# Performance work log

Measured on AMD Instinct MI355X. Metric: run time of the kernel, lower is better.

## Reference

```python
import jax, jax.numpy as jnp
import numpy as np

B, J, V, G, D = 1, 24, 20000, 2, 3
DCIN = J * 12          # num_parts * (9 + 3)
DC = 4                 # d_cond
HID = 128
BETA = 100.0           # softplus beta
EPS = 1e-8


def softplus_b(x):
    return jax.nn.softplus(BETA * x) / BETA


def group_linear(x, W, b):
    # x: (J, N, din), W: (J, din, dout), b: (J, dout)
    return jnp.einsum('jnd,jdo->jno', x, W) + b[:, None, :]


def axis_angle_to_matrix(aa):
    # aa: (..., 3) -> (..., 3, 3), Rodrigues formula
    angle = jnp.linalg.norm(aa, axis=-1, keepdims=True)
    axis = aa / jnp.where(angle < 1e-12, 1.0, angle)
    x, y, z = axis[..., 0], axis[..., 1], axis[..., 2]
    a = angle[..., 0]
    c, s = jnp.cos(a), jnp.sin(a)
    C = 1.0 - c
    r0 = jnp.stack([c + x * x * C, x * y * C - z * s, x * z * C + y * s], axis=-1)
    r1 = jnp.stack([y * x * C + z * s, c + y * y * C, y * z * C - x * s], axis=-1)
    r2 = jnp.stack([z * x * C - y * s, z * y * C + x * s, c + z * z * C], axis=-1)
    return jnp.stack([r0, r1, r2], axis=-2)


def blending_weights(pts, Jtr_center, Jtr_neigh, Jtr_self, bid_this, bid_other, rigid_alpha, rigid_beta):
    # pts: (B,J,V,3); Jtr_*: (B,J,1,3); bid_*: (J,) int
    ra = jax.nn.elu(rigid_alpha - 1.0) + 1.0
    a_n = ra[bid_other, bid_this].reshape(1, -1, 1, 1)
    a_s = ra[bid_this, bid_other].reshape(1, -1, 1, 1)
    be_n = rigid_beta[bid_other, bid_this].reshape(1, -1, 1, 1)
    be_s = rigid_beta[bid_this, bid_other].reshape(1, -1, 1, 1)
    vec_bone_n = Jtr_neigh - Jtr_center
    vec_bone_s = Jtr_self - Jtr_center
    nb_n = jnp.linalg.norm(vec_bone_n, axis=-1, keepdims=True)
    nb_s = jnp.linalg.norm(vec_bone_s, axis=-1, keepdims=True)
    vb_n = (Jtr_neigh - Jtr_self) / (nb_n + nb_s + EPS) * nb_n
    vb_s = -vb_n / (nb_n + EPS) * nb_s
    n_n = jnp.linalg.norm(vb_n, axis=-1, keepdims=True)
    n_s = jnp.linalg.norm(vb_s, axis=-1, keepdims=True)
    tr_o = Jtr_neigh - vb_n
    vec_pts = jax.lax.stop_gradient(pts) - tr_o   # pts.detach() in torch
    d_n = vb_n / (n_n + EPS)
    d_s = vb_s / (n_s + EPS)
    r_n = jnp.sum(vec_pts * d_n, axis=-1, keepdims=True) / (n_n + EPS)
    r_s = jnp.sum(vec_pts * d_s, axis=-1, keepdims=True) / (n_s + EPS)
    return jax.nn.sigmoid((r_n * a_n + be_n) - (r_s * a_s + be_s))


def _forward(pts, Bcond, Btr, Brot, Bneigh, rigid_alpha, rigid_beta,
             cW0, cb0, cW1, cb1, cW2, cb2, W0, b0, W1, b1, W2, b2, W3, b3):
    # world -> per-part local coords: (B,J,V,3)
    Brot_inv = jnp.swapaxes(Brot, -1, -2)
    pts_local = jnp.einsum('bjxy,bjvy->bjvx', Brot_inv, pts[:, None] - Btr[:, :, None])
    # neighbor-based deformation offsets
    ids = jax.lax.stop_gradient(Bneigh[0, :, :, 4, :2]).astype(jnp.int32)  # (J,G,2)
    offset_sum = jnp.zeros_like(pts_local)
    for gi in range(G):  # small fixed neighbor count
        Jtr_this = Bneigh[:, :, gi, 0][:, :, None]    # (B,J,1,3)
        Jtr_center = Bneigh[:, :, gi, 1][:, :, None]
        Jtr_other = Bneigh[:, :, gi, 2][:, :, None]
        Jpose = Bneigh[:, :, gi, 3][:, :, None]
        w = blending_weights(pts_local, Jtr_center, Jtr_other, Jtr_this,
                             ids[:, gi, 0], ids[:, gi, 1], rigid_alpha, rigid_beta)  # (B,J,V,1)
        Jp_w = jnp.nan_to_num(Jpose * w)              # (B,J,V,3)
        R = axis_angle_to_matrix(-Jp_w)               # (B,J,V,3,3)
        off = jnp.einsum('bjvxy,bjvy->bjvx', R, pts_local - Jtr_center) + Jtr_center - pts_local
        offset_sum = offset_sum + jnp.nan_to_num(off)
    pts_local = pts_local + offset_sum
    # grouped per-part MLP (INR with num_groups=J)
    x_in = jnp.transpose(pts_local, (1, 0, 2, 3)).reshape(J, B * V, D)
    cond = jnp.broadcast_to(jnp.transpose(Bcond, (1, 0, 2))[:, :, None, :], (J, B, V, DCIN)).reshape(J, B * V, DCIN)
    c = softplus_b(group_linear(cond, cW0, cb0))
    c = softplus_b(group_linear(c, cW1, cb1))
    c = group_linear(c, cW2, cb2)                      # (J, BV, 4)
    x = jnp.concatenate([x_in, c], axis=-1)            # (J, BV, 7)
    x = softplus_b(group_linear(x, W0, b0))
    x = softplus_b(group_linear(x, W1, b1))
    x = softplus_b(group_linear(x, W2, b2))
    x = group_linear(x, W3, b3)                        # (J, BV, 1)
    pred_parts = jnp.transpose(x.reshape(J, B, V, 1), (1, 0, 2, 3))  # (B,J,V,1)
    # softmin blend over parts
    pred_min = jnp.min(pred_parts, axis=1)             # (B,V,1)
    delta = pred_parts - pred_min[:, None]
    wsm = jax.nn.softmax(-delta * 200.0, axis=1)       # Softmin(dim=1)
    return jnp.sum(delta * wsm, axis=1) + pred_min


def setup_inputs() -> dict:
    key = jax.random.key(0)
    ks = jax.random.split(key, 16)
    pts = jax.random.normal(ks[0], (B, V, D), jnp.float32)
    Bcond = jax.random.normal(ks[1], (B, J, DCIN), jnp.float32) * 0.1
    Btr = jax.random.normal(ks[2], (B, J, D), jnp.float32)
    Brot = jax.random.normal(ks[3], (B, J, D, D), jnp.float32)
    core = jax.random.normal(ks[4], (B, J, G, 4, D), jnp.float32) * 0.5
    ids_this = jnp.arange(J, dtype=jnp.float32)
    ids_o0 = jnp.mod(jnp.arange(J) + 1, J).astype(jnp.float32)
    ids_o1 = jnp.mod(jnp.arange(J) - 1, J).astype(jnp.float32)
    bid = jnp.zeros((B, J, G, 1, D), jnp.float32)
    bid = bid.at[:, :, 0, 0, 0].set(ids_this).at[:, :, 0, 0, 1].set(ids_o0)
    bid = bid.at[:, :, 1, 0, 0].set(ids_this).at[:, :, 1, 0, 1].set(ids_o1)
    Bneigh = jnp.concatenate([core, bid], axis=-2)     # (B,J,G,5,D)
    rigid_alpha = jnp.full((J, J), 2.0, jnp.float32)   # blend_alpha init
    rigid_beta = jnp.zeros((J, J), jnp.float32)
    def gl(k, din, dout, std):
        return jax.random.normal(k, (J, din, dout), jnp.float32) * std, jnp.zeros((J, dout), jnp.float32)
    cW0, cb0 = gl(ks[5], DCIN, DC * 4, float(np.sqrt(2.0 / DCIN)))
    cW1, cb1 = gl(ks[6], DC * 4, DC * 4, float(np.sqrt(2.0 / (DC * 4))))
    cW2, cb2 = gl(ks[7], DC * 4, DC, 1e-5)
    std_h = float(np.sqrt(2.0) / np.sqrt(HID))
    W0, b0 = gl(ks[8], D + DC, HID, std_h)
    W1, b1 = gl(ks[9], HID, HID, std_h)
    W2, b2 = gl(ks[10], HID, HID, std_h)
    W3 = jax.random.normal(ks[11], (J, HID, 1), jnp.float32) * 1e-5 + float(np.sqrt(np.pi) / np.sqrt(HID))
    b3 = jnp.full((J, 1), -1.0, jnp.float32)           # -radius_init
    return {'pts': pts, 'Bcond': Bcond, 'Btr': Btr, 'Brot': Brot, 'Bneigh': Bneigh,
            'rigid_alpha': rigid_alpha, 'rigid_beta': rigid_beta,
            'cW0': cW0, 'cb0': cb0, 'cW1': cW1, 'cb1': cb1, 'cW2': cW2, 'cb2': cb2,
            'W0': W0, 'b0': b0, 'W1': W1, 'b1': b1, 'W2': W2, 'b2': b2, 'W3': W3, 'b3': b3}


def reference(pts, Bcond, Btr, Brot, Bneigh, rigid_alpha, rigid_beta,
              cW0, cb0, cW1, cb1, cW2, cb2, W0, b0, W1, b1, W2, b2, W3, b3):
    return _forward(pts, Bcond, Btr, Brot, Bneigh, rigid_alpha, rigid_beta,
                    cW0, cb0, cW1, cb1, cW2, cb2, W0, b0, W1, b1, W2, b2, W3, b3)
```

## Files before the change

### kernel.cpp

```cpp
#include <hip/hip_runtime.h>
#include <hip/hip_bf16.h>
#include <math.h>

#define VN 20000
#define JN 24
#define TILE 64
#define KP 132
#define EPSF 1e-8f

typedef __attribute__((ext_vector_type(8))) short bfrag;
typedef __attribute__((ext_vector_type(4))) float f32x4;

#define WJ_STRIDE 73728
#define L0H 0
#define L0L 4096
#define L1H 8192
#define L1L 24576
#define L2H 40960
#define L2L 57344

__device__ __forceinline__ unsigned short f2bf(float x) {
    __hip_bfloat16 b = __float2bfloat16(x);
    unsigned short u; __builtin_memcpy(&u, &b, 2); return u;
}
__device__ __forceinline__ float bf2f(unsigned short u) {
    __hip_bfloat16 b; __builtin_memcpy(&b, &u, 2);
    return __bfloat162float(b);
}
__device__ __forceinline__ unsigned int pack_hl(float x) {
    const unsigned int ux = __float_as_uint(x) + 0x8000u;
    const unsigned int h  = ux & 0xffff0000u;
    const float lo = x - __uint_as_float(h);
    const unsigned int ul = __float_as_uint(lo) + 0x8000u;
    return (h >> 16) | (ul & 0xffff0000u);
}

__device__ __forceinline__ float softplus_fast(float x) {
    const float u = __expf(-100.0f * fabsf(x));
    const float y = 2.0f * u - 1.0f;
    float p = fmaf(y, 0.0009515f, -0.0034665f);
    p = fmaf(y, p, 0.0122786f);
    p = fmaf(y, p, -0.0554079f);
    p = fmaf(y, p, 0.3333420f);
    p = fmaf(y, p, 0.4054545f);
    return fmaf(0.01f, p, fmaxf(x, 0.0f));
}

__global__ __launch_bounds__(384) void prep_kernel(
    const float* __restrict__ Bcond, const float* __restrict__ Bneigh,
    const float* __restrict__ ralpha, const float* __restrict__ rbeta,
    const float* __restrict__ cW0, const float* __restrict__ cb0,
    const float* __restrict__ cW1, const float* __restrict__ cb1,
    const float* __restrict__ cW2, const float* __restrict__ cb2,
    float* __restrict__ c4, float* __restrict__ geom)
{
    __shared__ float hbuf[JN][16];
    const int t = threadIdx.x;

    if (t < JN * 2) {
        const int j = t >> 1, gi = t & 1;
        const float* nb = Bneigh + (j * 2 + gi) * 15;
        const float tx = nb[0],  ty = nb[1],  tz = nb[2];
        const float cx = nb[3],  cy = nb[4],  cz = nb[5];
        const float ox = nb[6],  oy = nb[7],  oz = nb[8];
        const float px = nb[9],  py = nb[10], pz = nb[11];
        const int bid_this  = (int)nb[12];
        const int bid_other = (int)nb[13];
        const float xa_n = ralpha[bid_other * JN + bid_this] - 1.0f;
        const float xa_s = ralpha[bid_this * JN + bid_other] - 1.0f;
        const float a_n = xa_n > 0.0f ? xa_n + 1.0f : expf(xa_n);
        const float a_s = xa_s > 0.0f ? xa_s + 1.0f : expf(xa_s);
        const float be_n = rbeta[bid_other * JN + bid_this];
        const float be_s = rbeta[bid_this * JN + bid_other];

        const float bnx = ox - cx, bny = oy - cy, bnz = oz - cz;
        const float bsx = tx - cx, bsy = ty - cy, bsz = tz - cz;
        const float nb_n = sqrtf(bnx*bnx + bny*bny + bnz*bnz);
        const float nb_s = sqrtf(bsx*bsx + bsy*bsy + bsz*bsz);
        const float f = nb_n / (nb_n + nb_s + EPSF);
        const float vbnx = (ox - tx) * f, vbny = (oy - ty) * f, vbnz = (oz - tz) * f;
        const float g2 = -nb_s / (nb_n + EPSF);
        const float vbsx = vbnx * g2, vbsy = vbny * g2, vbsz = vbnz * g2;
        const float n_n = sqrtf(vbnx*vbnx + vbny*vbny + vbnz*vbnz);
        const float n_s = sqrtf(vbsx*vbsx + vbsy*vbsy + vbsz*vbsz);
        const float trx = ox - vbnx, tr_y = oy - vbny, trz = oz - vbnz;
        const float inn = 1.0f / ((n_n + EPSF) * (n_n + EPSF));
        const float ins = 1.0f / ((n_s + EPSF) * (n_s + EPSF));
        const float gx = vbnx * inn * a_n - vbsx * ins * a_s;
        const float gy = vbny * inn * a_n - vbsy * ins * a_s;
        const float gz = vbnz * inn * a_n - vbsz * ins * a_s;
        const float h = -(trx * gx + tr_y * gy + trz * gz) + be_n - be_s;
        float* gm = geom + (j * 2 + gi) * 12;
        gm[0] = gx; gm[1] = gy; gm[2] = gz; gm[3] = h;
        gm[4] = px; gm[5] = py; gm[6] = pz;
        gm[7] = cx; gm[8] = cy; gm[9] = cz;
        gm[10] = 0.0f; gm[11] = 0.0f;
    }

    {
        const int j = t >> 4, o = t & 15;
        const float* cond = Bcond + j * 288;
        const float* w = cW0 + j * 288 * 16 + o;
        float acc = cb0[j * 16 + o];
        for (int d = 0; d < 288; ++d) acc = fmaf(cond[d], w[d * 16], acc);
        hbuf[j][o] = softplus_fast(acc);
    }
    __syncthreads();
    {
        const int j = t >> 4, o = t & 15;
        const float* w = cW1 + j * 256 + o;
        float acc = cb1[j * 16 + o];
        #pragma unroll
        for (int d = 0; d < 16; ++d) acc = fmaf(hbuf[j][d], w[d * 16], acc);
        acc = softplus_fast(acc);
        __syncthreads();
        hbuf[j][o] = acc;
    }
    __syncthreads();
    if (t < JN * 4) {
        const int j = t >> 2, o = t & 3;
        const float* w = cW2 + j * 64 + o;
        float acc = cb2[j * 4 + o];
        #pragma unroll
        for (int d = 0; d < 16; ++d) acc = fmaf(hbuf[j][d], w[d * 4], acc);
        c4[j * 4 + o] = acc;
    }
}

__global__ __launch_bounds__(256) void wprep_kernel(
    const float* __restrict__ W0, const float* __restrict__ W1,
    const float* __restrict__ W2, unsigned short* __restrict__ wt)
{
    const int g = blockIdx.x * 256 + threadIdx.x;
    const int jj = g / 36864;
    const int r = g - jj * 36864;
    const float* src; int idx, kin, hoff, loff;
    if (r < 4096)       { idx = r;         kin = 7;   src = W0 + jj * 896;   hoff = L0H; loff = L0L; }
    else if (r < 20480) { idx = r - 4096;  kin = 128; src = W1 + jj * 16384; hoff = L1H; loff = L1L; }
    else                { idx = r - 20480; kin = 128; src = W2 + jj * 16384; hoff = L2H; loff = L2L; }
    const int j8   = idx & 7;
    const int lane = (idx >> 3) & 63;
    const int nt   = (idx >> 9) & 7;
    const int ks   = idx >> 12;
    const int n = nt * 16 + (lane & 15);
    const int k = ks * 32 + (lane >> 4) * 8 + j8;
    const float v = (k < kin) ? src[k * 128 + n] : 0.0f;
    const unsigned short h = f2bf(v);
    const unsigned short l = f2bf(v - bf2f(h));
    unsigned short* dj = wt + jj * WJ_STRIDE;
    dj[hoff + idx] = h;
    dj[loff + idx] = l;
}

__device__ __forceinline__ void mfma_layer(
    unsigned int* __restrict__ X,
    const unsigned short* __restrict__ wh,
    const unsigned short* __restrict__ wl,
    const float* __restrict__ bvec,
    int q, int lane, int nks)
{
    const int l = lane & 15;
    const int quad = lane >> 4;
    const float bia0 = bvec[q * 32 + l];
    const float bia1 = bvec[q * 32 + 16 + l];
    f32x4 acc[4][2];
    #pragma unroll
    for (int mi = 0; mi < 4; ++mi) {
        acc[mi][0] = (f32x4){bia0, bia0, bia0, bia0};
        acc[mi][1] = (f32x4){bia1, bia1, bia1, bia1};
    }

    #pragma unroll 1
    for (int ks = 0; ks < nks; ++ks) {
        bfrag bh[2], bl[2];
        #pragma unroll
        for (int ni = 0; ni < 2; ++ni) {
            const int off = ((ks * 8 + (q * 2 + ni)) * 64 + lane) * 8;
            bh[ni] = *(const bfrag*)(wh + off);
            bl[ni] = *(const bfrag*)(wl + off);
        }
        #pragma unroll
        for (int mi = 0; mi < 4; ++mi) {
            const unsigned int* ap = X + (mi * 16 + l) * KP + ks * 32 + quad * 8;
            union { uint4 v[2]; unsigned int u[8]; } d;
            d.v[0] = *(const uint4*)ap;
            d.v[1] = *(const uint4*)(ap + 4);
            union { unsigned int u[4]; bfrag f; } ah, al;
            #pragma unroll
            for (int jj = 0; jj < 4; ++jj) {
                ah.u[jj] = __builtin_amdgcn_perm(d.u[2*jj+1], d.u[2*jj], 0x05040100u);
                al.u[jj] = __builtin_amdgcn_perm(d.u[2*jj+1], d.u[2*jj], 0x07060302u);
            }
            #pragma unroll
            for (int ni = 0; ni < 2; ++ni) {
                acc[mi][ni] = __builtin_amdgcn_mfma_f32_16x16x32_bf16(ah.f, bh[ni], acc[mi][ni], 0, 0, 0);
                acc[mi][ni] = __builtin_amdgcn_mfma_f32_16x16x32_bf16(al.f, bh[ni], acc[mi][ni], 0, 0, 0);
                acc[mi][ni] = __builtin_amdgcn_mfma_f32_16x16x32_bf16(ah.f, bl[ni], acc[mi][ni], 0, 0, 0);
            }
        }
    }
    __syncthreads();
    #pragma unroll
    for (int ni = 0; ni < 2; ++ni) {
        const int ch = q * 32 + ni * 16 + l;
        #pragma unroll
        for (int mi = 0; mi < 4; ++mi) {
            #pragma unroll
            for (int r = 0; r < 4; ++r) {
                const float v = softplus_fast(acc[mi][ni][r]);
                const int p = mi * 16 + quad * 4 + r;
                X[p * KP + ch] = pack_hl(v);
            }
        }
    }
    __syncthreads();
}

__global__ __launch_bounds__(256, 4) void main_kernel(
    const float* __restrict__ pts, const float* __restrict__ Btr,
    const float* __restrict__ Brot,
    const float* __restrict__ b0, const float* __restrict__ b1,
    const float* __restrict__ b2, const float* __restrict__ W3,
    const float* __restrict__ b3,
    const float* __restrict__ c4, const float* __restrict__ geom,
    const unsigned short* __restrict__ wt,
    float* __restrict__ pred)
{
    __shared__ unsigned int X[TILE * KP];
    const int j = blockIdx.y;
    const int v0 = blockIdx.x * TILE;
    const int t = threadIdx.x;
    const int lane = t & 63;
    const int q = __builtin_amdgcn_readfirstlane(t >> 6);

    if (t < TILE) {
        const int v = v0 + t;
        float plx = 0.0f, ply = 0.0f, plz = 0.0f;
        if (v < VN) {
            const float dx = pts[v * 3 + 0] - Btr[j * 3 + 0];
            const float dy = pts[v * 3 + 1] - Btr[j * 3 + 1];
            const float dz = pts[v * 3 + 2] - Btr[j * 3 + 2];
            const float* R = Brot + j * 9;
            plx = R[0] * dx + R[3] * dy + R[6] * dz;
            ply = R[1] * dx + R[4] * dy + R[7] * dz;
            plz = R[2] * dx + R[5] * dy + R[8] * dz;
            float osx = 0.0f, osy = 0.0f, osz = 0.0f;
            #pragma unroll
            for (int gi = 0; gi < 2; ++gi) {
                const float* gm = geom + (j * 2 + gi) * 12;
                const float arg = plx * gm[0] + ply * gm[1] + plz * gm[2] + gm[3];
                const float w = 1.0f / (1.0f + __expf(-arg));
                const float aax = -gm[4] * w, aay = -gm[5] * w, aaz = -gm[6] * w;
                const float jcx = gm[7], jcy = gm[8], jcz = gm[9];
                const float ang = sqrtf(aax * aax + aay * aay + aaz * aaz);
                const float inv = ang < 1e-12f ? 1.0f : 1.0f / ang;
                const float ux = aax * inv, uy = aay * inv, uz = aaz * inv;
                const float co = __cosf(ang), si = __sinf(ang), C = 1.0f - co;
                const float vx = plx - jcx, vy = ply - jcy, vz = plz - jcz;
                const float du = ux * vx + uy * vy + uz * vz;
                const float cxv = uy * vz - uz * vy;
                const float cyv = uz * vx - ux * vz;
                const float czv = ux * vy - uy * vx;
                float offx = co * vx + si * cxv + C * ux * du + jcx - plx;
                float offy = co * vy + si * cyv + C * uy * du + jcy - ply;
                float offz = co * vz + si * czv + C * uz * du + jcz - plz;
                if (isnan(offx)) offx = 0.0f;
                if (isnan(offy)) offy = 0.0f;
                if (isnan(offz)) offz = 0.0f;
                osx += offx; osy += offy; osz += offz;
            }
            plx += osx; ply += osy; plz += osz;
        }
        X[t * KP + 0] = pack_hl(plx);
        X[t * KP + 1] = pack_hl(ply);
        X[t * KP + 2] = pack_hl(plz);
        X[t * KP + 3] = pack_hl(c4[j * 4 + 0]);
        X[t * KP + 4] = pack_hl(c4[j * 4 + 1]);
        X[t * KP + 5] = pack_hl(c4[j * 4 + 2]);
        X[t * KP + 6] = pack_hl(c4[j * 4 + 3]);
        #pragma unroll
        for (int k = 7; k < 32; ++k) X[t * KP + k] = 0u;
    }
    __syncthreads();

    const unsigned short* wj = wt + j * WJ_STRIDE;
    mfma_layer(X, wj + L0H, wj + L0L, b0 + j * 128, q, lane, 1);
    mfma_layer(X, wj + L1H, wj + L1L, b1 + j * 128, q, lane, 4);
    mfma_layer(X, wj + L2H, wj + L2L, b2 + j * 128, q, lane, 4);

    {
        const float* w3 = W3 + j * 128 + q * 32;
        float part = 0.0f;
        #pragma unroll 8
        for (int kk = 0; kk < 32; ++kk) {
            const unsigned int d = X[lane * KP + q * 32 + kk];
            const float xv = __uint_as_float(d << 16)
                           + __uint_as_float(d & 0xffff0000u);
            part = fmaf(xv, w3[kk], part);
        }
        X[lane * KP + 128 + q] = __float_as_uint(part);
    }
    __syncthreads();
    if (t < TILE) {
        const int v = v0 + t;
        const float r = b3[j]
            + __uint_as_float(X[t * KP + 128]) + __uint_as_float(X[t * KP + 129])
            + __uint_as_float(X[t * KP + 130]) + __uint_as_float(X[t * KP + 131]);
        if (v < VN) pred[j * VN + v] = r;
    }
}

__global__ __launch_bounds__(256) void softmin_kernel(const float* __restrict__ pred,
                                                      float* __restrict__ out)
{
    const int v = blockIdx.x * 256 + threadIdx.x;
    if (v >= VN) return;
    float vals[JN];
    float m = 3.4e38f;
    #pragma unroll
    for (int jj = 0; jj < JN; ++jj) {
        vals[jj] = pred[jj * VN + v];
        m = fminf(m, vals[jj]);
    }
    float s1 = 0.0f, s2 = 0.0f;
    #pragma unroll
    for (int jj = 0; jj < JN; ++jj) {
        const float d = vals[jj] - m;
        const float e = __expf(-200.0f * d);
        s1 += e;
        s2 = fmaf(d, e, s2);
    }
    out[v] = s2 / s1 + m;
}

extern "C" void kernel_launch(void* const* d_in, const int* in_sizes, int n_in,
                              void* d_out, int out_size, void* d_ws, size_t ws_size,
                              hipStream_t stream)
{
    const float* pts    = (const float*)d_in[0];
    const float* Bcond  = (const float*)d_in[1];
    const float* Btr    = (const float*)d_in[2];
    const float* Brot   = (const float*)d_in[3];
    const float* Bneigh = (const float*)d_in[4];
    const float* ralpha = (const float*)d_in[5];
    const float* rbeta  = (const float*)d_in[6];
    const float* cW0 = (const float*)d_in[7];
    const float* cb0 = (const float*)d_in[8];
    const float* cW1 = (const float*)d_in[9];
    const float* cb1 = (const float*)d_in[10];
    const float* cW2 = (const float*)d_in[11];
    const float* cb2 = (const float*)d_in[12];
    const float* W0 = (const float*)d_in[13];
    const float* b0 = (const float*)d_in[14];
    const float* W1 = (const float*)d_in[15];
    const float* b1 = (const float*)d_in[16];
    const float* W2 = (const float*)d_in[17];
    const float* b2 = (const float*)d_in[18];
    const float* W3 = (const float*)d_in[19];
    const float* b3 = (const float*)d_in[20];

    float* ws   = (float*)d_ws;
    float* pred = ws;
    float* c4   = ws + JN * VN;
    float* geom = c4 + JN * 4;
    unsigned short* wt = (unsigned short*)(geom + JN * 2 * 12);

    prep_kernel<<<1, 384, 0, stream>>>(Bcond, Bneigh, ralpha, rbeta,
                                       cW0, cb0, cW1, cb1, cW2, cb2, c4, geom);

    wprep_kernel<<<(JN * 36864) / 256, 256, 0, stream>>>(W0, W1, W2, wt);

    dim3 grid((VN + TILE - 1) / TILE, JN);
    main_kernel<<<grid, 256, 0, stream>>>(pts, Btr, Brot,
                                          b0, b1, b2, W3, b3,
                                          c4, geom, wt, pred);

    softmin_kernel<<<(VN + 255) / 256, 256, 0, stream>>>(pred, (float*)d_out);
}
```

Baseline: 257.3 us.

## Fold split-bf16 activations into doubled K dimension, cutting MFMAs from three to two

Activations are kept as interleaved (hi, lo) bf16 pairs, so the A fragment is read straight from LDS with no perm unpacking. The weights are laid out with K doubled: one matrix holds the hi weight for both hi and lo activations, and a second holds the lo weight for the hi slot and zero for the lo slot. Each k-step now issues two MFMAs instead of three, but the K loop runs twice as many steps and the weight buffer is larger. Softplus is also rewritten with exp2 and a different polynomial, and the hi/lo packing now uses the v_cvt_pk_bf16_f32 instruction.

```diff
diff --git a/kernel.cpp b/kernel.cpp
--- a/kernel.cpp
+++ b/kernel.cpp
@@ -11,13 +11,13 @@
 typedef __attribute__((ext_vector_type(8))) short bfrag;
 typedef __attribute__((ext_vector_type(4))) float f32x4;
 
-#define WJ_STRIDE 73728
-#define L0H 0
-#define L0L 4096
-#define L1H 8192
-#define L1L 24576
-#define L2H 40960
-#define L2L 57344
+#define WJ_STRIDE 139264
+#define L0A 0
+#define L0B 4096
+#define L1A 8192
+#define L1B 40960
+#define L2A 73728
+#define L2B 106496
 
 __device__ __forceinline__ unsigned short f2bf(float x) {
     __hip_bfloat16 b = __float2bfloat16(x);
@@ -28,22 +28,22 @@
     return __bfloat162float(b);
 }
 __device__ __forceinline__ unsigned int pack_hl(float x) {
-    const unsigned int ux = __float_as_uint(x) + 0x8000u;
-    const unsigned int h  = ux & 0xffff0000u;
-    const float lo = x - __uint_as_float(h);
-    const unsigned int ul = __float_as_uint(lo) + 0x8000u;
-    return (h >> 16) | (ul & 0xffff0000u);
+    const unsigned int h = (__float_as_uint(x) + 0x8000u) & 0xffff0000u;
+    const float hf = __uint_as_float(h);
+    const float lo = x - hf;
+    unsigned int r;
+    asm("v_cvt_pk_bf16_f32 %0, %1, %2" : "=v"(r) : "v"(hf), "v"(lo));
+    return r;
 }
 
 __device__ __forceinline__ float softplus_fast(float x) {
-    const float u = __expf(-100.0f * fabsf(x));
-    const float y = 2.0f * u - 1.0f;
-    float p = fmaf(y, 0.0009515f, -0.0034665f);
-    p = fmaf(y, p, 0.0122786f);
-    p = fmaf(y, p, -0.0554079f);
-    p = fmaf(y, p, 0.3333420f);
-    p = fmaf(y, p, 0.4054545f);
-    return fmaf(0.01f, p, fmaxf(x, 0.0f));
+    const float u = __builtin_amdgcn_exp2f(-144.269504f * fabsf(x));
+    float p = fmaf(u, 3.04480e-4f, -1.31584e-3f);
+    p = fmaf(u, p, 2.852768e-3f);
+    p = fmaf(u, p, -4.902308e-3f);
+    p = fmaf(u, p, 9.992342e-3f);
+    p = fmaf(u, p, 8.0e-8f);
+    return fmaxf(x, 0.0f) + p;
 }
 
 __global__ __launch_bounds__(384) void prep_kernel(
@@ -132,30 +132,31 @@
     const float* __restrict__ W2, unsigned short* __restrict__ wt)
 {
     const int g = blockIdx.x * 256 + threadIdx.x;
-    const int jj = g / 36864;
-    const int r = g - jj * 36864;
-    const float* src; int idx, kin, hoff, loff;
-    if (r < 4096)       { idx = r;         kin = 7;   src = W0 + jj * 896;   hoff = L0H; loff = L0L; }
-    else if (r < 20480) { idx = r - 4096;  kin = 128; src = W1 + jj * 16384; hoff = L1H; loff = L1L; }
-    else                { idx = r - 20480; kin = 128; src = W2 + jj * 16384; hoff = L2H; loff = L2L; }
-    const int j8   = idx & 7;
-    const int lane = (idx >> 3) & 63;
-    const int nt   = (idx >> 9) & 7;
-    const int ks   = idx >> 12;
+    const int jj = g / WJ_STRIDE;
+    const int r = g - jj * WJ_STRIDE;
+    const float* src; int kin, pr; bool loP;
+    if (r < 8192)       { src = W0 + jj * 896;   kin = 7;   pr = r & 4095;            loP = r >= L0B; }
+    else if (r < 73728) { src = W1 + jj * 16384; kin = 128; pr = (r - L1A) & 32767;   loP = r >= L1B; }
+    else                { src = W2 + jj * 16384; kin = 128; pr = (r - L2A) & 32767;   loP = r >= L2B; }
+    const int j8   = pr & 7;
+    const int lane = (pr >> 3) & 63;
+    const int nt   = (pr >> 9) & 7;
+    const int ks   = pr >> 12;
     const int n = nt * 16 + (lane & 15);
-    const int k = ks * 32 + (lane >> 4) * 8 + j8;
+    const int kext = ks * 32 + (lane >> 4) * 8 + j8;
+    const int k = kext >> 1;
     const float v = (k < kin) ? src[k * 128 + n] : 0.0f;
     const unsigned short h = f2bf(v);
-    const unsigned short l = f2bf(v - bf2f(h));
-    unsigned short* dj = wt + jj * WJ_STRIDE;
-    dj[hoff + idx] = h;
-    dj[loff + idx] = l;
+    unsigned short outv;
+    if (!loP) outv = h;
+    else      outv = (kext & 1) ? (unsigned short)0 : f2bf(v - bf2f(h));
+    wt[jj * WJ_STRIDE + r] = outv;
 }
 
 __device__ __forceinline__ void mfma_layer(
     unsigned int* __restrict__ X,
-    const unsigned short* __restrict__ wh,
-    const unsigned short* __restrict__ wl,
+    const unsigned short* __restrict__ wA,
+    const unsigned short* __restrict__ wB,
     const float* __restrict__ bvec,
     int q, int lane, int nks)
 {
@@ -172,30 +173,21 @@
 
     #pragma unroll 1
     for (int ks = 0; ks < nks; ++ks) {
-        bfrag bh[2], bl[2];
+        bfrag bA[2], bB[2];
         #pragma unroll
         for (int ni = 0; ni < 2; ++ni) {
             const int off = ((ks * 8 + (q * 2 + ni)) * 64 + lane) * 8;
-            bh[ni] = *(const bfrag*)(wh + off);
-            bl[ni] = *(const bfrag*)(wl + off);
+            bA[ni] = *(const bfrag*)(wA + off);
+            bB[ni] = *(const bfrag*)(wB + off);
         }
         #pragma unroll
         for (int mi = 0; mi < 4; ++mi) {
-            const unsigned int* ap = X + (mi * 16 + l) * KP + ks * 32 + quad * 8;
-            union { uint4 v[2]; unsigned int u[8]; } d;
-            d.v[0] = *(const uint4*)ap;
-            d.v[1] = *(const uint4*)(ap + 4);
-            union { unsigned int u[4]; bfrag f; } ah, al;
-            #pragma unroll
-            for (int jj = 0; jj < 4; ++jj) {
-                ah.u[jj] = __builtin_amdgcn_perm(d.u[2*jj+1], d.u[2*jj], 0x05040100u);
-                al.u[jj] = __builtin_amdgcn_perm(d.u[2*jj+1], d.u[2*jj], 0x07060302u);
-            }
+            const bfrag a = *(const bfrag*)(
+                (const unsigned short*)(X + (mi * 16 + l) * KP) + ks * 32 + quad * 8);
             #pragma unroll
             for (int ni = 0; ni < 2; ++ni) {
-                acc[mi][ni] = __builtin_amdgcn_mfma_f32_16x16x32_bf16(ah.f, bh[ni], acc[mi][ni], 0, 0, 0);
-                acc[mi][ni] = __builtin_amdgcn_mfma_f32_16x16x32_bf16(al.f, bh[ni], acc[mi][ni], 0, 0, 0);
-                acc[mi][ni] = __builtin_amdgcn_mfma_f32_16x16x32_bf16(ah.f, bl[ni], acc[mi][ni], 0, 0, 0);
+                acc[mi][ni] = __builtin_amdgcn_mfma_f32_16x16x32_bf16(a, bA[ni], acc[mi][ni], 0, 0, 0);
+                acc[mi][ni] = __builtin_amdgcn_mfma_f32_16x16x32_bf16(a, bB[ni], acc[mi][ni], 0, 0, 0);
             }
         }
     }
@@ -279,14 +271,14 @@
         X[t * KP + 5] = pack_hl(c4[j * 4 + 2]);
         X[t * KP + 6] = pack_hl(c4[j * 4 + 3]);
         #pragma unroll
-        for (int k = 7; k < 32; ++k) X[t * KP + k] = 0u;
+        for (int k = 7; k < 16; ++k) X[t * KP + k] = 0u;
     }
     __syncthreads();
 
     const unsigned short* wj = wt + j * WJ_STRIDE;
-    mfma_layer(X, wj + L0H, wj + L0L, b0 + j * 128, q, lane, 1);
-    mfma_layer(X, wj + L1H, wj + L1L, b1 + j * 128, q, lane, 4);
-    mfma_layer(X, wj + L2H, wj + L2L, b2 + j * 128, q, lane, 4);
+    mfma_layer(X, wj + L0A, wj + L0B, b0 + j * 128, q, lane, 1);
+    mfma_layer(X, wj + L1A, wj + L1B, b1 + j * 128, q, lane, 8);
+    mfma_layer(X, wj + L2A, wj + L2B, b2 + j * 128, q, lane, 8);
 
     {
         const float* w3 = W3 + j * 128 + q * 32;
@@ -368,7 +360,7 @@
     prep_kernel<<<1, 384, 0, stream>>>(Bcond, Bneigh, ralpha, rbeta,
                                        cW0, cb0, cW1, cb1, cW2, cb2, c4, geom);
 
-    wprep_kernel<<<(JN * 36864) / 256, 256, 0, stream>>>(W0, W1, W2, wt);
+    wprep_kernel<<<(JN * WJ_STRIDE) / 256, 256, 0, stream>>>(W0, W1, W2, wt);
 
     dim3 grid((VN + TILE - 1) / TILE, JN);
     main_kernel<<<grid, 256, 0, stream>>>(pts, Btr, Brot,
```

New measurement: 269.2 us. 1.05x slower.
